# Performance work log

Hardware: AMD Instinct MI355X
Metric: run time of the kernel (lower is better)

Reference implementation:

```python
import jax, jax.numpy as jnp
import numpy as np

BATCH = 32768
TEXT_DIM = 384
HIDDEN = 256
NUM_LAYERS = 4
NUM_VERTS = 12
K_NN = 6


def _build_template():
    """Icosphere vertices (12, normalized) and row-normalized kNN adjacency (12,12)."""
    phi = (1.0 + 5.0 ** 0.5) / 2.0
    v = np.array([
        [-1, phi, 0], [1, phi, 0], [-1, -phi, 0], [1, -phi, 0],
        [0, -1, phi], [0, 1, phi], [0, -1, -phi], [0, 1, -phi],
        [phi, 0, -1], [phi, 0, 1], [-phi, 0, -1], [-phi, 0, 1],
    ], dtype=np.float32)
    v = v / np.linalg.norm(v, axis=1, keepdims=True)
    dist = np.linalg.norm(v[:, None, :] - v[None, :, :], axis=-1)  # (12,12)
    # k+1 smallest per row; index 0 is self (distance 0), skip it
    idx = np.argsort(dist, axis=1, kind='stable')[:, 1:K_NN + 1]
    adj = np.zeros((NUM_VERTS, NUM_VERTS), dtype=np.float32)
    rows = np.repeat(np.arange(NUM_VERTS), K_NN)
    adj[rows, idx.reshape(-1)] = 1.0
    adj = adj / (adj.sum(axis=1, keepdims=True) + 1e-6)
    return jnp.asarray(v), jnp.asarray(adj)


def setup_inputs() -> dict:
    key = jax.random.key(0)
    ks = jax.random.split(key, 8)
    template, adjacency = _build_template()
    scale = 0.02
    return {
        "text_emb": jax.random.normal(ks[0], (BATCH, TEXT_DIM), dtype=jnp.float32),
        "W_text": jax.random.normal(ks[1], (TEXT_DIM, HIDDEN), dtype=jnp.float32) * scale,
        "b_text": jnp.zeros((HIDDEN,), dtype=jnp.float32),
        "W_gnn": jax.random.normal(ks[2], (NUM_LAYERS, HIDDEN, HIDDEN), dtype=jnp.float32) * scale,
        "b_gnn": jnp.zeros((NUM_LAYERS, HIDDEN), dtype=jnp.float32),
        "W_out": jax.random.normal(ks[3], (HIDDEN, 3), dtype=jnp.float32) * scale,
        "b_out": jnp.zeros((3,), dtype=jnp.float32),
        "adjacency": adjacency,   # (12,12) buffer
        "template": template,     # (12,3) buffer
    }


def reference(text_emb, W_text, b_text, W_gnn, b_gnn, W_out, b_out, adjacency, template):
    # text projection -> broadcast to all nodes
    tf = text_emb @ W_text + b_text                       # (B, H)
    B = text_emb.shape[0]
    h = jnp.broadcast_to(tf[:, None, :], (B, NUM_VERTS, HIDDEN))
    # GNN layers: aggregate (shared adjacency across batch), project, relu
    for l in range(NUM_LAYERS):
        agg = jnp.einsum('nm,bmd->bnd', adjacency, h)     # (B, 12, H)
        h = jax.nn.relu(agg @ W_gnn[l] + b_gnn[l])
    displacements = h @ W_out + b_out                     # (B, 12, 3)
    return template[None, :, :] + displacements
```

## Files before the change

### kernel.cpp

```cpp
#include <hip/hip_runtime.h>
#include <stdint.h>

#define TD      384
#define HID     256
#define NLAYERS 4
#define ROWB    528

typedef __bf16 bf16;
typedef __attribute__((ext_vector_type(8))) __bf16 bf16x8;
typedef __attribute__((ext_vector_type(4))) float f32x4;

union FragU { uint4 u; bf16x8 f; };
union PackU { uint4 u; bf16 v[8]; };

__device__ inline f32x4 mfma16(bf16x8 a, bf16x8 b, f32x4 c) {
  return __builtin_amdgcn_mfma_f32_16x16x32_bf16(a, b, c, 0, 0, 0);
}

__global__ __launch_bounds__(256) void prep_kernel(
    const float* __restrict__ W_text, const float* __restrict__ W_gnn,
    const float* __restrict__ W_out,
    bf16* __restrict__ wt_text, bf16* __restrict__ wt_gnn, float* __restrict__ wot)
{
  int bid = blockIdx.x, tid = threadIdx.x;
  if (bid < 48) {
    int idx = bid * 256 + tid;
    int cc = idx & 15, c = idx >> 4;
    int n16 = c / 48, oct = c - n16 * 48;
    int n = n16 * 16 + cc;
    PackU pk;
    #pragma unroll
    for (int j = 0; j < 8; j++) pk.v[j] = (bf16)W_text[(oct * 8 + j) * HID + n];
    *(uint4*)(wt_text + idx * 8) = pk.u;
  } else if (bid < 176) {
    int idx = (bid - 48) * 256 + tid;
    int cc = idx & 15, c = idx >> 4;
    int l = c >> 9, c2 = c & 511;
    int oct = c2 & 31;
    int n = (c2 >> 5) * 16 + cc;
    const float* base = W_gnn + l * HID * HID;
    PackU pk;
    #pragma unroll
    for (int j = 0; j < 8; j++) pk.v[j] = (bf16)base[(oct * 8 + j) * HID + n];
    *(uint4*)(wt_gnn + idx * 8) = pk.u;
  } else {
    for (int t = tid; t < 3 * HID; t += 256) {
      int comp = t >> 8, k = t & 255;
      wot[comp * HID + k] = W_out[k * 3 + comp];
    }
  }
}

__global__ __launch_bounds__(256, 2) void mesh_kernel(
    const float* __restrict__ text,
    const bf16* __restrict__ wt_text,
    const bf16* __restrict__ wt_gnn,
    const float* __restrict__ b_text,
    const float* __restrict__ b_gnn,
    const float* __restrict__ wot,
    const float* __restrict__ b_out,
    const float* __restrict__ tmpl,
    float* __restrict__ out)
{
  __shared__ __align__(16) unsigned char smem[2 * 64 * ROWB];
  unsigned char* hb0 = smem;
  unsigned char* hb1 = smem + 64 * ROWB;

  const int tid  = threadIdx.x;
  const int lane = tid & 63;
  const int w    = tid >> 6;
  const int cc   = lane & 15;
  const int qq   = lane >> 4;
  const int mh   = w >> 1;
  const int nh   = w & 1;
  const int rowbase = blockIdx.x * 64;
  const int voff = qq * 256 + cc * 16;

  f32x4 acc[2][8];

  auto zero_acc = [&]() {
    f32x4 z = {0.f, 0.f, 0.f, 0.f};
    #pragma unroll
    for (int mt = 0; mt < 2; mt++)
      #pragma unroll
      for (int nt = 0; nt < 8; nt++) acc[mt][nt] = z;
  };

  auto loadB = [&](const char* wbase, int ks, bf16x8* B, int K8x256) {
    #pragma unroll
    for (int nt = 0; nt < 8; nt++) {
      FragU fu; fu.u = *(const uint4*)(wbase + ks * 1024 + nt * K8x256);
      B[nt] = fu.f;
    }
  };

  auto loadA = [&](const unsigned char* src, int ks, bf16x8* A) {
    #pragma unroll
    for (int mt = 0; mt < 2; mt++) {
      int m = mh * 32 + mt * 16 + cc;
      FragU fu; fu.u = *(const uint4*)(src + m * ROWB + ks * 64 + qq * 16);
      A[mt] = fu.f;
    }
  };

  auto loadAtext = [&](int ks, bf16x8* A) {
    #pragma unroll
    for (int mt = 0; mt < 2; mt++) {
      int row = rowbase + mh * 32 + mt * 16 + cc;
      const float4* p = (const float4*)(text + row * TD + ks * 32 + qq * 8);
      float4 x = p[0], y = p[1];
      bf16x8 f;
      f[0]=(bf16)x.x; f[1]=(bf16)x.y; f[2]=(bf16)x.z; f[3]=(bf16)x.w;
      f[4]=(bf16)y.x; f[5]=(bf16)y.y; f[6]=(bf16)y.z; f[7]=(bf16)y.w;
      A[mt] = f;
    }
  };

  auto write_h = [&](unsigned char* dst, const float* bias_ptr, bool relu) {
    float bias[8];
    #pragma unroll
    for (int nt = 0; nt < 8; nt++) bias[nt] = bias_ptr[nh * 128 + nt * 16 + cc];
    #pragma unroll
    for (int mt = 0; mt < 2; mt++) {
      #pragma unroll
      for (int nt = 0; nt < 8; nt++) {
        int col = nh * 128 + nt * 16 + cc;
        #pragma unroll
        for (int r = 0; r < 4; r++) {
          int m = mh * 32 + mt * 16 + qq * 4 + r;
          float v = acc[mt][nt][r] + bias[nt];
          if (relu) v = fmaxf(v, 0.f);
          *(bf16*)(dst + m * ROWB + col * 2) = (bf16)v;
        }
      }
    }
  };

  {
    const char* wbase = (const char*)wt_text + nh * 8 * 12288 + voff;
    zero_acc();
    bf16x8 A[2], B[8];
    loadB(wbase, 0, B, 12288);
    loadAtext(0, A);
    #pragma unroll
    for (int ks = 0; ks < TD / 32; ks++) {
      bf16x8 An[2], Bn[8];
      if (ks + 1 < TD / 32) { loadB(wbase, ks + 1, Bn, 12288); loadAtext(ks + 1, An); }
      #pragma unroll
      for (int nt = 0; nt < 8; nt++) {
        acc[0][nt] = mfma16(A[0], B[nt], acc[0][nt]);
        acc[1][nt] = mfma16(A[1], B[nt], acc[1][nt]);
      }
      if (ks + 1 < TD / 32) {
        #pragma unroll
        for (int nt = 0; nt < 8; nt++) B[nt] = Bn[nt];
        A[0] = An[0]; A[1] = An[1];
      }
    }
    write_h(hb0, b_text, false);
  }
  __syncthreads();

  for (int l = 0; l < NLAYERS; l++) {
    const unsigned char* src = (l & 1) ? hb1 : hb0;
    unsigned char*       dst = (l & 1) ? hb0 : hb1;
    const char* wbase = (const char*)(wt_gnn + l * HID * HID) + nh * 8 * 8192 + voff;
    zero_acc();
    bf16x8 A[2], B[8];
    loadB(wbase, 0, B, 8192);
    loadA(src, 0, A);
    #pragma unroll
    for (int ks = 0; ks < HID / 32; ks++) {
      bf16x8 An[2], Bn[8];
      if (ks + 1 < HID / 32) { loadB(wbase, ks + 1, Bn, 8192); loadA(src, ks + 1, An); }
      #pragma unroll
      for (int nt = 0; nt < 8; nt++) {
        acc[0][nt] = mfma16(A[0], B[nt], acc[0][nt]);
        acc[1][nt] = mfma16(A[1], B[nt], acc[1][nt]);
      }
      if (ks + 1 < HID / 32) {
        #pragma unroll
        for (int nt = 0; nt < 8; nt++) B[nt] = Bn[nt];
        A[0] = An[0]; A[1] = An[1];
      }
    }
    write_h(dst, b_gnn + l * HID, l < NLAYERS - 1 ? true : true);
    __syncthreads();
  }

  float* dispBuf = (float*)hb1;

  if (tid < 192) {
    int comp = tid >> 6;
    int r = tid & 63;
    const float4* wrow = (const float4*)(wot + comp * HID);
    float s = 0.f;
    #pragma unroll 4
    for (int o = 0; o < 32; o++) {
      FragU fu; fu.u = *(const uint4*)(hb0 + r * ROWB + o * 16);
      float4 w0 = wrow[2 * o], w1 = wrow[2 * o + 1];
      s += (float)fu.f[0]*w0.x + (float)fu.f[1]*w0.y + (float)fu.f[2]*w0.z + (float)fu.f[3]*w0.w;
      s += (float)fu.f[4]*w1.x + (float)fu.f[5]*w1.y + (float)fu.f[6]*w1.z + (float)fu.f[7]*w1.w;
    }
    dispBuf[r * 3 + comp] = s + b_out[comp];
  }
  __syncthreads();

  #pragma unroll
  for (int ii = 0; ii < 9; ii++) {
    int i = ii * 256 + tid;
    int row = i / 36;
    int j = i - row * 36;
    out[rowbase * 36 + i] = tmpl[j] + dispBuf[row * 3 + j % 3];
  }
}

extern "C" void kernel_launch(void* const* d_in, const int* in_sizes, int n_in,
                              void* d_out, int out_size, void* d_ws, size_t ws_size,
                              hipStream_t stream) {
  const float* text   = (const float*)d_in[0];
  const float* W_text = (const float*)d_in[1];
  const float* b_text = (const float*)d_in[2];
  const float* W_gnn  = (const float*)d_in[3];
  const float* b_gnn  = (const float*)d_in[4];
  const float* W_out  = (const float*)d_in[5];
  const float* b_out  = (const float*)d_in[6];
  const float* tmpl   = (const float*)d_in[8];
  float* outp = (float*)d_out;

  bf16* wt_text = (bf16*)d_ws;
  bf16* wt_gnn  = wt_text + 256*384;
  float* wot    = (float*)(wt_gnn + 4*256*256);

  prep_kernel<<<177, 256, 0, stream>>>(W_text, W_gnn, W_out, wt_text, wt_gnn, wot);
  mesh_kernel<<<32768/64, 256, 0, stream>>>(text, wt_text, wt_gnn, b_text, b_gnn,
                                            wot, b_out, tmpl, outp);
}
```

Before: 139.0 us.

## Stage text tile in LDS, use XOR-swizzled layout, and retile warps to full rows

The 64x384 text tile is now loaded cooperatively and converted to bf16 into LDS once, instead of each warp converting strided global rows inside the K loop. Warps now each own 64 output columns across all 64 rows (4x4 MFMA tiles) instead of a 2x2 row/column split, so every weight fragment is loaded from global once per block. The padded row layout is replaced by an XOR swizzle to avoid LDS bank conflicts. LDS use grows to 80 KB per block, which with launch bounds of 2 blocks may cut occupancy on this hardware.

```diff
diff --git a/kernel.cpp b/kernel.cpp
--- a/kernel.cpp
+++ b/kernel.cpp
@@ -4,7 +4,6 @@
 #define TD      384
 #define HID     256
 #define NLAYERS 4
-#define ROWB    528
 
 typedef __bf16 bf16;
 typedef __attribute__((ext_vector_type(8))) __bf16 bf16x8;
@@ -62,133 +61,120 @@
     const float* __restrict__ tmpl,
     float* __restrict__ out)
 {
-  __shared__ __align__(16) unsigned char smem[2 * 64 * ROWB];
-  unsigned char* hb0 = smem;
-  unsigned char* hb1 = smem + 64 * ROWB;
+  __shared__ __align__(16) unsigned char smem[81920];
+  unsigned char* Tbuf = smem;
+  unsigned char* Hbuf = smem + 49152;
 
   const int tid  = threadIdx.x;
   const int lane = tid & 63;
   const int w    = tid >> 6;
   const int cc   = lane & 15;
   const int qq   = lane >> 4;
-  const int mh   = w >> 1;
-  const int nh   = w & 1;
   const int rowbase = blockIdx.x * 64;
-  const int voff = qq * 256 + cc * 16;
-
-  f32x4 acc[2][8];
+
+  f32x4 acc[4][4];
+
+  {
+    const float* tbase = text + (size_t)rowbase * TD;
+    #pragma unroll
+    for (int i = 0; i < 12; i++) {
+      int id = i * 256 + tid;
+      int m = id / 48, o = id - m * 48;
+      const float4* p = (const float4*)(tbase + m * TD + o * 8);
+      float4 x = p[0], y = p[1];
+      PackU pk;
+      pk.v[0]=(bf16)x.x; pk.v[1]=(bf16)x.y; pk.v[2]=(bf16)x.z; pk.v[3]=(bf16)x.w;
+      pk.v[4]=(bf16)y.x; pk.v[5]=(bf16)y.y; pk.v[6]=(bf16)y.z; pk.v[7]=(bf16)y.w;
+      *(uint4*)(Tbuf + m * 768 + (o ^ (m & 7)) * 16) = pk.u;
+    }
+  }
+  __syncthreads();
 
   auto zero_acc = [&]() {
     f32x4 z = {0.f, 0.f, 0.f, 0.f};
     #pragma unroll
-    for (int mt = 0; mt < 2; mt++)
+    for (int mt = 0; mt < 4; mt++)
       #pragma unroll
-      for (int nt = 0; nt < 8; nt++) acc[mt][nt] = z;
-  };
-
-  auto loadB = [&](const char* wbase, int ks, bf16x8* B, int K8x256) {
-    #pragma unroll
-    for (int nt = 0; nt < 8; nt++) {
-      FragU fu; fu.u = *(const uint4*)(wbase + ks * 1024 + nt * K8x256);
+      for (int nt = 0; nt < 4; nt++) acc[mt][nt] = z;
+  };
+
+  auto loadA = [&](const unsigned char* src, int rowB, int ks, bf16x8* A) {
+    #pragma unroll
+    for (int mt = 0; mt < 4; mt++) {
+      int m = mt * 16 + cc;
+      FragU fu;
+      fu.u = *(const uint4*)(src + m * rowB + (((ks * 4 + qq) ^ (m & 7)) * 16));
+      A[mt] = fu.f;
+    }
+  };
+
+  auto loadB = [&](const char* wb, int K8, int ks, bf16x8* B) {
+    #pragma unroll
+    for (int nt = 0; nt < 4; nt++) {
+      FragU fu;
+      fu.u = *(const uint4*)(wb + (size_t)(nt * K8 + ks * 4) * 256);
       B[nt] = fu.f;
     }
   };
 
-  auto loadA = [&](const unsigned char* src, int ks, bf16x8* A) {
-    #pragma unroll
-    for (int mt = 0; mt < 2; mt++) {
-      int m = mh * 32 + mt * 16 + cc;
-      FragU fu; fu.u = *(const uint4*)(src + m * ROWB + ks * 64 + qq * 16);
-      A[mt] = fu.f;
-    }
-  };
-
-  auto loadAtext = [&](int ks, bf16x8* A) {
-    #pragma unroll
-    for (int mt = 0; mt < 2; mt++) {
-      int row = rowbase + mh * 32 + mt * 16 + cc;
-      const float4* p = (const float4*)(text + row * TD + ks * 32 + qq * 8);
-      float4 x = p[0], y = p[1];
-      bf16x8 f;
-      f[0]=(bf16)x.x; f[1]=(bf16)x.y; f[2]=(bf16)x.z; f[3]=(bf16)x.w;
-      f[4]=(bf16)y.x; f[5]=(bf16)y.y; f[6]=(bf16)y.z; f[7]=(bf16)y.w;
-      A[mt] = f;
-    }
-  };
-
-  auto write_h = [&](unsigned char* dst, const float* bias_ptr, bool relu) {
-    float bias[8];
-    #pragma unroll
-    for (int nt = 0; nt < 8; nt++) bias[nt] = bias_ptr[nh * 128 + nt * 16 + cc];
-    #pragma unroll
-    for (int mt = 0; mt < 2; mt++) {
+  auto runLayer = [&](const unsigned char* src, int rowB, int nks,
+                      const char* wb, int K8,
+                      unsigned char* dst, const float* bias_ptr, bool relu) {
+    zero_acc();
+    bf16x8 A[4], B[4], An[4], Bn[4];
+    loadB(wb, K8, 0, B);
+    loadA(src, rowB, 0, A);
+    #pragma unroll
+    for (int ks = 0; ks < nks; ks++) {
+      if (ks + 1 < nks) {
+        loadB(wb, K8, ks + 1, Bn);
+        loadA(src, rowB, ks + 1, An);
+      }
       #pragma unroll
-      for (int nt = 0; nt < 8; nt++) {
-        int col = nh * 128 + nt * 16 + cc;
+      for (int mt = 0; mt < 4; mt++)
+        #pragma unroll
+        for (int nt = 0; nt < 4; nt++)
+          acc[mt][nt] = mfma16(A[mt], B[nt], acc[mt][nt]);
+      if (ks + 1 < nks) {
+        #pragma unroll
+        for (int t = 0; t < 4; t++) { A[t] = An[t]; B[t] = Bn[t]; }
+      }
+    }
+    float bias4[4];
+    #pragma unroll
+    for (int nt = 0; nt < 4; nt++) bias4[nt] = bias_ptr[w * 64 + nt * 16 + cc];
+    #pragma unroll
+    for (int mt = 0; mt < 4; mt++) {
+      #pragma unroll
+      for (int nt = 0; nt < 4; nt++) {
+        int col = w * 64 + nt * 16 + cc;
         #pragma unroll
         for (int r = 0; r < 4; r++) {
-          int m = mh * 32 + mt * 16 + qq * 4 + r;
-          float v = acc[mt][nt][r] + bias[nt];
+          int m = mt * 16 + qq * 4 + r;
+          float v = acc[mt][nt][r] + bias4[nt];
           if (relu) v = fmaxf(v, 0.f);
-          *(bf16*)(dst + m * ROWB + col * 2) = (bf16)v;
+          *(bf16*)(dst + m * 512 + ((col >> 3) ^ (m & 7)) * 16 + (col & 7) * 2) = (bf16)v;
         }
       }
     }
   };
 
-  {
-    const char* wbase = (const char*)wt_text + nh * 8 * 12288 + voff;
-    zero_acc();
-    bf16x8 A[2], B[8];
-    loadB(wbase, 0, B, 12288);
-    loadAtext(0, A);
-    #pragma unroll
-    for (int ks = 0; ks < TD / 32; ks++) {
-      bf16x8 An[2], Bn[8];
-      if (ks + 1 < TD / 32) { loadB(wbase, ks + 1, Bn, 12288); loadAtext(ks + 1, An); }
-      #pragma unroll
-      for (int nt = 0; nt < 8; nt++) {
-        acc[0][nt] = mfma16(A[0], B[nt], acc[0][nt]);
-        acc[1][nt] = mfma16(A[1], B[nt], acc[1][nt]);
-      }
-      if (ks + 1 < TD / 32) {
-        #pragma unroll
-        for (int nt = 0; nt < 8; nt++) B[nt] = Bn[nt];
-        A[0] = An[0]; A[1] = An[1];
-      }
-    }
-    write_h(hb0, b_text, false);
-  }
+  const char* wb0 = (const char*)wt_text + (size_t)(w * 4 * 48 + qq) * 256 + cc * 16;
+
+  runLayer(Tbuf, 768, TD / 32, wb0, 48, Hbuf, b_text, false);
   __syncthreads();
 
+  #pragma unroll
   for (int l = 0; l < NLAYERS; l++) {
-    const unsigned char* src = (l & 1) ? hb1 : hb0;
-    unsigned char*       dst = (l & 1) ? hb0 : hb1;
-    const char* wbase = (const char*)(wt_gnn + l * HID * HID) + nh * 8 * 8192 + voff;
-    zero_acc();
-    bf16x8 A[2], B[8];
-    loadB(wbase, 0, B, 8192);
-    loadA(src, 0, A);
-    #pragma unroll
-    for (int ks = 0; ks < HID / 32; ks++) {
-      bf16x8 An[2], Bn[8];
-      if (ks + 1 < HID / 32) { loadB(wbase, ks + 1, Bn, 8192); loadA(src, ks + 1, An); }
-      #pragma unroll
-      for (int nt = 0; nt < 8; nt++) {
-        acc[0][nt] = mfma16(A[0], B[nt], acc[0][nt]);
-        acc[1][nt] = mfma16(A[1], B[nt], acc[1][nt]);
-      }
-      if (ks + 1 < HID / 32) {
-        #pragma unroll
-        for (int nt = 0; nt < 8; nt++) B[nt] = Bn[nt];
-        A[0] = An[0]; A[1] = An[1];
-      }
-    }
-    write_h(dst, b_gnn + l * HID, l < NLAYERS - 1 ? true : true);
+    const unsigned char* src = (l & 1) ? Tbuf : Hbuf;
+    unsigned char*       dst = (l & 1) ? Hbuf : Tbuf;
+    const char* wb = (const char*)(wt_gnn) + (size_t)l * HID * HID * 2
+                   + (size_t)(w * 4 * 32 + qq) * 256 + cc * 16;
+    runLayer(src, 512, HID / 32, wb, 32, dst, b_gnn + l * HID, true);
     __syncthreads();
   }
 
-  float* dispBuf = (float*)hb1;
+  float* dispBuf = (float*)Tbuf;
 
   if (tid < 192) {
     int comp = tid >> 6;
@@ -197,7 +183,7 @@
     float s = 0.f;
     #pragma unroll 4
     for (int o = 0; o < 32; o++) {
-      FragU fu; fu.u = *(const uint4*)(hb0 + r * ROWB + o * 16);
+      FragU fu; fu.u = *(const uint4*)(Hbuf + r * 512 + ((o ^ (r & 7)) * 16));
       float4 w0 = wrow[2 * o], w1 = wrow[2 * o + 1];
       s += (float)fu.f[0]*w0.x + (float)fu.f[1]*w0.y + (float)fu.f[2]*w0.z + (float)fu.f[3]*w0.w;
       s += (float)fu.f[4]*w1.x + (float)fu.f[5]*w1.y + (float)fu.f[6]*w1.z + (float)fu.f[7]*w1.w;
@@ -211,7 +197,7 @@
     int i = ii * 256 + tid;
     int row = i / 36;
     int j = i - row * 36;
-    out[rowbase * 36 + i] = tmpl[j] + dispBuf[row * 3 + j % 3];
+    out[(size_t)rowbase * 36 + i] = tmpl[j] + dispBuf[row * 3 + j % 3];
   }
 }
 
```

New measurement: 124.8 us. 10.2% less time.

## Use 8 waves per block with narrower wave tiles and XOR-swizzled LDS rows

Applied to the files above, without the earlier changes.

Doubles the block from 256 to 512 threads. Each wave now computes a 32x64 output tile instead of 32x128, so accumulator and B-fragment registers shrink and more waves run per CU. The padded 528-byte LDS rows are replaced by 512-byte rows with an XOR swizzle on 16-byte chunks to avoid bank conflicts while fitting two 32KB buffers. The cost is more A-fragment LDS reads per block and a tight register budget from the launch bound, which could cause spills.

```diff
diff --git a/kernel.cpp b/kernel.cpp
--- a/kernel.cpp
+++ b/kernel.cpp
@@ -4,7 +4,6 @@
 #define TD      384
 #define HID     256
 #define NLAYERS 4
-#define ROWB    528
 
 typedef __bf16 bf16;
 typedef __attribute__((ext_vector_type(8))) __bf16 bf16x8;
@@ -51,7 +50,7 @@
   }
 }
 
-__global__ __launch_bounds__(256, 2) void mesh_kernel(
+__global__ __launch_bounds__(512, 4) void mesh_kernel(
     const float* __restrict__ text,
     const bf16* __restrict__ wt_text,
     const bf16* __restrict__ wt_gnn,
@@ -62,34 +61,34 @@
     const float* __restrict__ tmpl,
     float* __restrict__ out)
 {
-  __shared__ __align__(16) unsigned char smem[2 * 64 * ROWB];
+  __shared__ __align__(16) unsigned char smem[65536];
   unsigned char* hb0 = smem;
-  unsigned char* hb1 = smem + 64 * ROWB;
+  unsigned char* hb1 = smem + 32768;
 
   const int tid  = threadIdx.x;
   const int lane = tid & 63;
   const int w    = tid >> 6;
+  const int mh   = w >> 2;
+  const int nc   = w & 3;
   const int cc   = lane & 15;
   const int qq   = lane >> 4;
-  const int mh   = w >> 1;
-  const int nh   = w & 1;
   const int rowbase = blockIdx.x * 64;
-  const int voff = qq * 256 + cc * 16;
-
-  f32x4 acc[2][8];
+
+  f32x4 acc[2][4];
 
   auto zero_acc = [&]() {
     f32x4 z = {0.f, 0.f, 0.f, 0.f};
     #pragma unroll
     for (int mt = 0; mt < 2; mt++)
       #pragma unroll
-      for (int nt = 0; nt < 8; nt++) acc[mt][nt] = z;
-  };
-
-  auto loadB = [&](const char* wbase, int ks, bf16x8* B, int K8x256) {
-    #pragma unroll
-    for (int nt = 0; nt < 8; nt++) {
-      FragU fu; fu.u = *(const uint4*)(wbase + ks * 1024 + nt * K8x256);
+      for (int nt = 0; nt < 4; nt++) acc[mt][nt] = z;
+  };
+
+  auto loadB = [&](const char* wb, int K8, int ks, bf16x8* B) {
+    #pragma unroll
+    for (int nt = 0; nt < 4; nt++) {
+      FragU fu;
+      fu.u = *(const uint4*)(wb + (size_t)(nt * K8 + ks * 4) * 256);
       B[nt] = fu.f;
     }
   };
@@ -98,7 +97,8 @@
     #pragma unroll
     for (int mt = 0; mt < 2; mt++) {
       int m = mh * 32 + mt * 16 + cc;
-      FragU fu; fu.u = *(const uint4*)(src + m * ROWB + ks * 64 + qq * 16);
+      FragU fu;
+      fu.u = *(const uint4*)(src + m * 512 + (((ks * 4 + qq) ^ (m & 7)) * 16));
       A[mt] = fu.f;
     }
   };
@@ -107,7 +107,7 @@
     #pragma unroll
     for (int mt = 0; mt < 2; mt++) {
       int row = rowbase + mh * 32 + mt * 16 + cc;
-      const float4* p = (const float4*)(text + row * TD + ks * 32 + qq * 8);
+      const float4* p = (const float4*)(text + (size_t)row * TD + ks * 32 + qq * 8);
       float4 x = p[0], y = p[1];
       bf16x8 f;
       f[0]=(bf16)x.x; f[1]=(bf16)x.y; f[2]=(bf16)x.z; f[3]=(bf16)x.w;
@@ -117,74 +117,74 @@
   };
 
   auto write_h = [&](unsigned char* dst, const float* bias_ptr, bool relu) {
-    float bias[8];
-    #pragma unroll
-    for (int nt = 0; nt < 8; nt++) bias[nt] = bias_ptr[nh * 128 + nt * 16 + cc];
+    float bias4[4];
+    #pragma unroll
+    for (int nt = 0; nt < 4; nt++) bias4[nt] = bias_ptr[nc * 64 + nt * 16 + cc];
     #pragma unroll
     for (int mt = 0; mt < 2; mt++) {
       #pragma unroll
-      for (int nt = 0; nt < 8; nt++) {
-        int col = nh * 128 + nt * 16 + cc;
+      for (int nt = 0; nt < 4; nt++) {
+        int col = nc * 64 + nt * 16 + cc;
         #pragma unroll
         for (int r = 0; r < 4; r++) {
           int m = mh * 32 + mt * 16 + qq * 4 + r;
-          float v = acc[mt][nt][r] + bias[nt];
+          float v = acc[mt][nt][r] + bias4[nt];
           if (relu) v = fmaxf(v, 0.f);
-          *(bf16*)(dst + m * ROWB + col * 2) = (bf16)v;
+          *(bf16*)(dst + m * 512 + ((col >> 3) ^ (m & 7)) * 16 + (col & 7) * 2) = (bf16)v;
         }
       }
     }
   };
 
   {
-    const char* wbase = (const char*)wt_text + nh * 8 * 12288 + voff;
+    const char* wb = (const char*)wt_text + (size_t)(nc * 4 * 48 + qq) * 256 + cc * 16;
     zero_acc();
-    bf16x8 A[2], B[8];
-    loadB(wbase, 0, B, 12288);
+    bf16x8 A[2], B[4], An[2], Bn[4];
+    loadB(wb, 48, 0, B);
     loadAtext(0, A);
     #pragma unroll
     for (int ks = 0; ks < TD / 32; ks++) {
-      bf16x8 An[2], Bn[8];
-      if (ks + 1 < TD / 32) { loadB(wbase, ks + 1, Bn, 12288); loadAtext(ks + 1, An); }
-      #pragma unroll
-      for (int nt = 0; nt < 8; nt++) {
-        acc[0][nt] = mfma16(A[0], B[nt], acc[0][nt]);
-        acc[1][nt] = mfma16(A[1], B[nt], acc[1][nt]);
+      if (ks + 1 < TD / 32) { loadB(wb, 48, ks + 1, Bn); loadAtext(ks + 1, An); }
+      #pragma unroll
+      for (int mt = 0; mt < 2; mt++)
+        #pragma unroll
+        for (int nt = 0; nt < 4; nt++)
+          acc[mt][nt] = mfma16(A[mt], B[nt], acc[mt][nt]);
+      if (ks + 1 < TD / 32) {
+        A[0] = An[0]; A[1] = An[1];
+        #pragma unroll
+        for (int t = 0; t < 4; t++) B[t] = Bn[t];
       }
-      if (ks + 1 < TD / 32) {
-        #pragma unroll
-        for (int nt = 0; nt < 8; nt++) B[nt] = Bn[nt];
-        A[0] = An[0]; A[1] = An[1];
-      }
     }
     write_h(hb0, b_text, false);
   }
   __syncthreads();
 
+  #pragma unroll
   for (int l = 0; l < NLAYERS; l++) {
     const unsigned char* src = (l & 1) ? hb1 : hb0;
     unsigned char*       dst = (l & 1) ? hb0 : hb1;
-    const char* wbase = (const char*)(wt_gnn + l * HID * HID) + nh * 8 * 8192 + voff;
+    const char* wb = (const char*)(wt_gnn) + (size_t)l * HID * HID * 2
+                   + (size_t)(nc * 4 * 32 + qq) * 256 + cc * 16;
     zero_acc();
-    bf16x8 A[2], B[8];
-    loadB(wbase, 0, B, 8192);
+    bf16x8 A[2], B[4], An[2], Bn[4];
+    loadB(wb, 32, 0, B);
     loadA(src, 0, A);
     #pragma unroll
     for (int ks = 0; ks < HID / 32; ks++) {
-      bf16x8 An[2], Bn[8];
-      if (ks + 1 < HID / 32) { loadB(wbase, ks + 1, Bn, 8192); loadA(src, ks + 1, An); }
-      #pragma unroll
-      for (int nt = 0; nt < 8; nt++) {
-        acc[0][nt] = mfma16(A[0], B[nt], acc[0][nt]);
-        acc[1][nt] = mfma16(A[1], B[nt], acc[1][nt]);
+      if (ks + 1 < HID / 32) { loadB(wb, 32, ks + 1, Bn); loadA(src, ks + 1, An); }
+      #pragma unroll
+      for (int mt = 0; mt < 2; mt++)
+        #pragma unroll
+        for (int nt = 0; nt < 4; nt++)
+          acc[mt][nt] = mfma16(A[mt], B[nt], acc[mt][nt]);
+      if (ks + 1 < HID / 32) {
+        A[0] = An[0]; A[1] = An[1];
+        #pragma unroll
+        for (int t = 0; t < 4; t++) B[t] = Bn[t];
       }
-      if (ks + 1 < HID / 32) {
-        #pragma unroll
-        for (int nt = 0; nt < 8; nt++) B[nt] = Bn[nt];
-        A[0] = An[0]; A[1] = An[1];
-      }
-    }
-    write_h(dst, b_gnn + l * HID, l < NLAYERS - 1 ? true : true);
+    }
+    write_h(dst, b_gnn + l * HID, true);
     __syncthreads();
   }
 
@@ -197,7 +197,7 @@
     float s = 0.f;
     #pragma unroll 4
     for (int o = 0; o < 32; o++) {
-      FragU fu; fu.u = *(const uint4*)(hb0 + r * ROWB + o * 16);
+      FragU fu; fu.u = *(const uint4*)(hb0 + r * 512 + ((o ^ (r & 7)) * 16));
       float4 w0 = wrow[2 * o], w1 = wrow[2 * o + 1];
       s += (float)fu.f[0]*w0.x + (float)fu.f[1]*w0.y + (float)fu.f[2]*w0.z + (float)fu.f[3]*w0.w;
       s += (float)fu.f[4]*w1.x + (float)fu.f[5]*w1.y + (float)fu.f[6]*w1.z + (float)fu.f[7]*w1.w;
@@ -206,12 +206,10 @@
   }
   __syncthreads();
 
-  #pragma unroll
-  for (int ii = 0; ii < 9; ii++) {
-    int i = ii * 256 + tid;
+  for (int i = tid; i < 2304; i += 512) {
     int row = i / 36;
     int j = i - row * 36;
-    out[rowbase * 36 + i] = tmpl[j] + dispBuf[row * 3 + j % 3];
+    out[(size_t)rowbase * 36 + i] = tmpl[j] + dispBuf[row * 3 + j % 3];
   }
 }
 
@@ -233,6 +231,6 @@
   float* wot    = (float*)(wt_gnn + 4*256*256);
 
   prep_kernel<<<177, 256, 0, stream>>>(W_text, W_gnn, W_out, wt_text, wt_gnn, wot);
-  mesh_kernel<<<32768/64, 256, 0, stream>>>(text, wt_text, wt_gnn, b_text, b_gnn,
-                                            wot, b_out, tmpl, outp);
-}
+  mesh_kernel<<<512, 512, 0, stream>>>(text, wt_text, wt_gnn, b_text, b_gnn,
+                                       wot, b_out, tmpl, outp);
+}
```

New measurement: 147.4 us. 1.06x slower.
